# Performance work log

Hardware: AMD Instinct MI355X
Metric: run time of the kernel (lower is better)

## Reference

```python
import jax, jax.numpy as jnp
import numpy as np

L, D, H, V, T_MAX, DFF = 8, 1024, 16, 50257, 1024, 4096
HS = D // H
EPS = 1e-5


def setup_inputs() -> dict:
    key = jax.random.key(0)
    ks = jax.random.split(key, 20)
    s = 0.02
    inp = {
        "idx": jax.random.randint(ks[0], (4, 1024), 0, V),
        "wte": jax.random.normal(ks[1], (V, D), jnp.float32) * s,
        "wpe": jax.random.normal(ks[2], (T_MAX, D), jnp.float32) * s,
        "wq": jax.random.normal(ks[3], (L, D, D), jnp.float32) * s,
        "wk": jax.random.normal(ks[4], (L, D, D), jnp.float32) * s,
        "wv": jax.random.normal(ks[5], (L, D, D), jnp.float32) * s,
        "wo": jax.random.normal(ks[6], (L, D, D), jnp.float32) * s,
        "bo": jnp.zeros((L, D), jnp.float32),
        "ln1_w": jnp.ones((L, D), jnp.float32),
        "ln1_b": jnp.zeros((L, D), jnp.float32),
        "ln2_w": jnp.ones((L, D), jnp.float32),
        "ln2_b": jnp.zeros((L, D), jnp.float32),
        "w1": jax.random.normal(ks[7], (L, D, DFF), jnp.float32) * s,
        "b1": jnp.zeros((L, DFF), jnp.float32),
        "w2": jax.random.normal(ks[8], (L, DFF, D), jnp.float32) * s,
        "b2": jnp.zeros((L, D), jnp.float32),
        "lnf_w": jnp.ones((D,), jnp.float32),
        "lnf_b": jnp.zeros((D,), jnp.float32),
        "wlm": jax.random.normal(ks[9], (D, V), jnp.float32) * s,
        "blm": jnp.zeros((V,), jnp.float32),
    }
    return inp


def _ln(x, w, b):
    mu = jnp.mean(x, axis=-1, keepdims=True)
    var = jnp.mean(jnp.square(x - mu), axis=-1, keepdims=True)
    return (x - mu) * jax.lax.rsqrt(var + EPS) * w + b


def _gpt_forward(idx, wte, wpe, wq, wk, wv, wo, bo, ln1_w, ln1_b, ln2_w, ln2_b,
                 w1, b1, w2, b2, lnf_w, lnf_b, wlm, blm):
    B, T = idx.shape
    x = wte[idx] + wpe[:T]                       # [B,T,D]
    causal = jnp.tril(jnp.ones((T, T), bool))    # same as tril buffer
    scale = HS ** -0.5
    for i in range(L):
        h = _ln(x, ln1_w[i], ln1_b[i])
        q = (h @ wq[i]).reshape(B, T, H, HS)
        k = (h @ wk[i]).reshape(B, T, H, HS)
        v = (h @ wv[i]).reshape(B, T, H, HS)
        wei = jnp.einsum('bqhd,bkhd->bhqk', q, k) * scale
        wei = jnp.where(causal, wei, -jnp.inf)
        wei = jax.nn.softmax(wei, axis=-1)
        attn = jnp.einsum('bhqk,bkhd->bqhd', wei, v).reshape(B, T, D)
        x = x + attn @ wo[i] + bo[i]
        h2 = _ln(x, ln2_w[i], ln2_b[i])
        x = x + jax.nn.relu(h2 @ w1[i] + b1[i]) @ w2[i] + b2[i]
    x = _ln(x, lnf_w, lnf_b)
    return x @ wlm + blm                          # logits [B,T,V]


def reference(idx, wte, wpe, wq, wk, wv, wo, bo, ln1_w, ln1_b, ln2_w, ln2_b,
              w1, b1, w2, b2, lnf_w, lnf_b, wlm, blm):
    return _gpt_forward(idx, wte, wpe, wq, wk, wv, wo, bo, ln1_w, ln1_b,
                        ln2_w, ln2_b, w1, b1, w2, b2, lnf_w, lnf_b, wlm, blm)
```

## Files before the change

kernel.cpp:

```cpp
#include <hip/hip_runtime.h>
#include <cstdint>
#include <cstddef>

typedef __attribute__((ext_vector_type(4))) float f32x4;
typedef __attribute__((ext_vector_type(8))) short s16x8;
typedef __attribute__((ext_vector_type(4))) unsigned short u16x4;
typedef __attribute__((ext_vector_type(2))) unsigned short u16x2;

#define NLAYER 8
#define DM 1024
#define NTOK 4096
#define DFF2 4096
#define NV 50257

__device__ __forceinline__ unsigned short f2bf(float f) {
  unsigned int u = __float_as_uint(f);
  u = u + 0x7fffu + ((u >> 16) & 1u);
  return (unsigned short)(u >> 16);
}

__device__ __forceinline__ void gload_lds16(const void* gp, void* lp) {
  const __attribute__((address_space(1))) unsigned int* g =
      reinterpret_cast<const __attribute__((address_space(1))) unsigned int*>(
          reinterpret_cast<uintptr_t>(gp));
  __attribute__((address_space(3))) unsigned int* l =
      reinterpret_cast<__attribute__((address_space(3))) unsigned int*>(
          (unsigned int)(uintptr_t)lp);
  __builtin_amdgcn_global_load_lds(g, l, 16, 0, 0);
}

__global__ void __launch_bounds__(256) convT_k(const float* __restrict__ in,
                                               unsigned short* __restrict__ out,
                                               int K, int N, size_t zStride) {
  __shared__ float tile[64][65];
  const int n0 = blockIdx.x * 64, k0 = blockIdx.y * 64;
  const float* inp = in + (size_t)blockIdx.z * K * N;
  unsigned short* outp = out + (size_t)blockIdx.z * zStride;
  const int tid = threadIdx.x;
#pragma unroll
  for (int p = 0; p < 16; ++p) {
    const int r = p * 4 + (tid >> 6);
    const int cc = tid & 63;
    const int gn = n0 + cc;
    tile[r][cc] = (gn < N) ? inp[(size_t)(k0 + r) * N + gn] : 0.f;
  }
  __syncthreads();
#pragma unroll
  for (int p = 0; p < 8; ++p) {
    const int lin = p * 256 + tid;
    const int rn = lin >> 5;
    const int c2 = (lin & 31) * 2;
    u16x2 o;
    o[0] = f2bf(tile[c2][rn]);
    o[1] = f2bf(tile[c2 + 1][rn]);
    *(u16x2*)&outp[(size_t)(n0 + rn) * K + k0 + c2] = o;
  }
}

__global__ void __launch_bounds__(256) embed_k(const int* __restrict__ idx,
                                               const float* __restrict__ wte,
                                               const float* __restrict__ wpe,
                                               float* __restrict__ X) {
  const int tok = blockIdx.x;
  const int t = tok & 1023;
  const int id = idx[tok];
  const int c = threadIdx.x * 4;
  f32x4 a = *(const f32x4*)&wte[(size_t)id * DM + c];
  f32x4 p = *(const f32x4*)&wpe[(size_t)t * DM + c];
  a = a + p;
  *(f32x4*)&X[(size_t)tok * DM + c] = a;
}

__global__ void __launch_bounds__(256) ln_k(const float* __restrict__ X,
                                            const float* __restrict__ W,
                                            const float* __restrict__ Bp,
                                            unsigned short* __restrict__ O) {
  const int row = blockIdx.x, tid = threadIdx.x;
  const size_t base = (size_t)row * DM;
  f32x4 v = *(const f32x4*)&X[base + tid * 4];
  float s = v[0] + v[1] + v[2] + v[3];
  float q = v[0] * v[0] + v[1] * v[1] + v[2] * v[2] + v[3] * v[3];
#pragma unroll
  for (int m = 1; m < 64; m <<= 1) {
    s += __shfl_xor(s, m);
    q += __shfl_xor(q, m);
  }
  __shared__ float ps[4], pq[4];
  const int wv = tid >> 6;
  if ((tid & 63) == 0) { ps[wv] = s; pq[wv] = q; }
  __syncthreads();
  s = ps[0] + ps[1] + ps[2] + ps[3];
  q = pq[0] + pq[1] + pq[2] + pq[3];
  const float mu = s * (1.f / DM);
  const float var = q * (1.f / DM) - mu * mu;
  const float rstd = rsqrtf(var + 1e-5f);
  f32x4 w = *(const f32x4*)&W[tid * 4];
  f32x4 bb = *(const f32x4*)&Bp[tid * 4];
  u16x4 o;
#pragma unroll
  for (int j = 0; j < 4; ++j) o[j] = f2bf((v[j] - mu) * rstd * w[j] + bb[j]);
  *(u16x4*)&O[base + tid * 4] = o;
}

__global__ void __launch_bounds__(256) reduce2ln_k(
    float* __restrict__ X, const float* __restrict__ bias,
    const float* __restrict__ P0, const float* __restrict__ P1,
    const float* __restrict__ W, const float* __restrict__ Bp,
    unsigned short* __restrict__ O) {
  const int row = blockIdx.x, tid = threadIdx.x;
  const size_t base = (size_t)row * DM;
  const size_t i = base + tid * 4;
  f32x4 v = *(f32x4*)&X[i];
  {
    f32x4 b = *(const f32x4*)&bias[tid * 4];
    f32x4 a = *(const f32x4*)&P0[i];
    f32x4 c = *(const f32x4*)&P1[i];
    v = v + b + a + c;
    *(f32x4*)&X[i] = v;
  }
  float s = v[0] + v[1] + v[2] + v[3];
  float q = v[0] * v[0] + v[1] * v[1] + v[2] * v[2] + v[3] * v[3];
#pragma unroll
  for (int m = 1; m < 64; m <<= 1) {
    s += __shfl_xor(s, m);
    q += __shfl_xor(q, m);
  }
  __shared__ float ps[4], pq[4];
  const int wv = tid >> 6;
  if ((tid & 63) == 0) { ps[wv] = s; pq[wv] = q; }
  __syncthreads();
  s = ps[0] + ps[1] + ps[2] + ps[3];
  q = pq[0] + pq[1] + pq[2] + pq[3];
  const float mu = s * (1.f / DM);
  const float var = q * (1.f / DM) - mu * mu;
  const float rstd = rsqrtf(var + 1e-5f);
  f32x4 w = *(const f32x4*)&W[tid * 4];
  f32x4 bb = *(const f32x4*)&Bp[tid * 4];
  u16x4 o;
#pragma unroll
  for (int j = 0; j < 4; ++j) o[j] = f2bf((v[j] - mu) * rstd * w[j] + bb[j]);
  *(u16x4*)&O[base + tid * 4] = o;
}

__global__ void __launch_bounds__(256) gemm_k(
    const unsigned short* __restrict__ A, const unsigned short* __restrict__ Bt,
    const float* __restrict__ bias, float* __restrict__ outF,
    unsigned short* __restrict__ outB, int M, int N, int K, int lda, int ldc) {
  __shared__ __align__(16) unsigned short lA[128 * 64];
  __shared__ __align__(16) unsigned short lB[128 * 64];
  const int tid = threadIdx.x;
  const int wv = tid >> 6, lane = tid & 63;
  const int row0 = blockIdx.y * 128, col0 = blockIdx.x * 128;
  const int wr = wv >> 1, wc = wv & 1;

  const int z = blockIdx.z;
  A += (size_t)z * K;
  Bt += (size_t)z * K;
  if (gridDim.z > 1) outF += (size_t)z * M * ldc;

  f32x4 acc[4][4] = {};

  const int sRow = tid >> 3;
  const int sColSw = ((tid & 7) * 8) ^ ((sRow & 7) * 8);
  const unsigned short* gA = A + (size_t)(row0 + sRow) * lda + sColSw;
  const unsigned short* gB = Bt + (size_t)(col0 + sRow) * lda + sColSw;
  unsigned short* lAd = lA + tid * 8;
  unsigned short* lBd = lB + tid * 8;
  const size_t step32 = (size_t)32 * lda;

  const int rbase = lane & 15;
  const int kHi = (lane >> 4) * 8;
  const int kSw = (lane & 7) * 8;

  for (int kt = 0; kt < K; kt += 64) {
#pragma unroll
    for (int i = 0; i < 4; ++i) {
      gload_lds16(gA + kt + i * step32, lAd + i * 2048);
      gload_lds16(gB + kt + i * step32, lBd + i * 2048);
    }
    __syncthreads();
    s16x8 af[2][4], bfr[2][4];
#pragma unroll
    for (int kk = 0; kk < 2; ++kk) {
      const int kph = (kk * 32 + kHi) ^ kSw;
#pragma unroll
      for (int m = 0; m < 4; ++m)
        af[kk][m] = *(const s16x8*)&lA[(wr * 64 + m * 16 + rbase) * 64 + kph];
#pragma unroll
      for (int n = 0; n < 4; ++n)
        bfr[kk][n] = *(const s16x8*)&lB[(wc * 64 + n * 16 + rbase) * 64 + kph];
    }
#pragma unroll
    for (int kk = 0; kk < 2; ++kk)
#pragma unroll
      for (int m = 0; m < 4; ++m)
#pragma unroll
        for (int n = 0; n < 4; ++n)
          acc[m][n] = __builtin_amdgcn_mfma_f32_16x16x32_bf16(
              af[kk][m], bfr[kk][n], acc[m][n], 0, 0, 0);
    __syncthreads();
  }

  const int baseRow = row0 + wr * 64 + ((lane >> 4) * 4);
  const int baseCol = col0 + wc * 64 + (lane & 15);
#pragma unroll
  for (int m = 0; m < 4; ++m) {
#pragma unroll
    for (int n = 0; n < 4; ++n) {
      const int colc = baseCol + n * 16;
      if (colc < N) {
        const float bv = bias ? bias[colc] : 0.f;
        const int rowc0 = baseRow + m * 16;
#pragma unroll
        for (int r = 0; r < 4; ++r) {
          float v = acc[m][n][r] + bv;
          if (outF) outF[(size_t)(rowc0 + r) * ldc + colc] = v;
          if (outB) outB[(size_t)(rowc0 + r) * ldc + colc] = f2bf(v);
        }
      }
    }
  }
}

__global__ void __launch_bounds__(512, 2) gemm8p_k(
    const unsigned short* __restrict__ A, const unsigned short* __restrict__ Bt,
    const float* __restrict__ bias, float* __restrict__ outF,
    unsigned short* __restrict__ outB, unsigned short* __restrict__ vt,
    int M, int N, int K, int lda, int ldc, int relu) {
  __shared__ __align__(16) unsigned short lA[2][2][8192];
  __shared__ __align__(16) unsigned short lB[2][2][8192];
  const int tid = threadIdx.x;
  const int wv = tid >> 6, lane = tid & 63;

  int bx = blockIdx.x, by = blockIdx.y;
  {
    const int nwg = gridDim.x * gridDim.y;
    if ((nwg & 7) == 0) {
      int lin = by * gridDim.x + bx;
      lin = (lin & 7) * (nwg >> 3) + (lin >> 3);
      by = lin / gridDim.x;
      bx = lin - by * gridDim.x;
    }
  }
  const int row0 = by * 256, col0 = bx * 256;
  const int wr = wv >> 2, wc = wv & 3;

  f32x4 acc[8][4] = {};

  const int sColSw = (((tid & 7) ^ ((tid >> 3) & 7))) * 8;
  const unsigned short* gA = A + (size_t)(row0 + (tid >> 3)) * lda + sColSw;
  const unsigned short* gB = Bt + (size_t)(col0 + (tid >> 3)) * lda + sColSw;
  const size_t step64 = (size_t)64 * lda;

  const int rbase = lane & 15;
  const int g8 = (lane >> 4) * 8;
  const int rsw = (rbase & 7) * 8;

  const int nt = K >> 6;

#define STGA(t, h)                                                       \
  {                                                                      \
    const unsigned short* s_ = gA + (size_t)(t) * 64 + (size_t)(2 * (h)) * step64; \
    gload_lds16(s_, &lA[(t) & 1][h][tid * 8]);                           \
    gload_lds16(s_ + step64, &lA[(t) & 1][h][4096 + tid * 8]);           \
  }
#define STGB(t, h)                                                       \
  {                                                                      \
    const unsigned short* s_ = gB + (size_t)(t) * 64 + (size_t)(2 * (h)) * step64; \
    gload_lds16(s_, &lB[(t) & 1][h][tid * 8]);                           \
    gload_lds16(s_ + step64, &lB[(t) & 1][h][4096 + tid * 8]);           \
  }

  STGA(0, 0); STGA(0, 1); STGB(0, 0); STGB(0, 1);
  STGA(1, 0); STGA(1, 1); STGB(1, 0);
  asm volatile("s_waitcnt vmcnt(6)" ::: "memory");
  __builtin_amdgcn_s_barrier();

  for (int t = 0; t < nt; ++t) {
    const int d = t & 1;
    const unsigned short* lah = &lA[d][wr][0];
    const unsigned short* lbh = &lB[d][wc >> 1][0];
    const int bro = (wc & 1) * 64;
    s16x8 af0[4][2], af1[4][2], bf01[2][2], bf23[2][2];
#pragma unroll
    for (int ks = 0; ks < 2; ++ks) {
      const int kph = (ks * 32 + g8) ^ rsw;
#pragma unroll
      for (int m = 0; m < 4; ++m)
        af0[m][ks] = *(const s16x8*)&lah[(m * 16 + rbase) * 64 + kph];
#pragma unroll
      for (int n = 0; n < 2; ++n)
        bf01[n][ks] = *(const s16x8*)&lbh[(bro + n * 16 + rbase) * 64 + kph];
    }
    if (t + 1 < nt) STGB(t + 1, 1);
    __builtin_amdgcn_s_barrier();
    asm volatile("s_waitcnt lgkmcnt(0)" ::: "memory");
    __builtin_amdgcn_s_setprio(1);
#pragma unroll
    for (int m = 0; m < 4; ++m)
#pragma unroll
      for (int n = 0; n < 2; ++n)
#pragma unroll
        for (int ks = 0; ks < 2; ++ks)
          acc[m][n] = __builtin_amdgcn_mfma_f32_16x16x32_bf16(
              af0[m][ks], bf01[n][ks], acc[m][n], 0, 0, 0);
    __builtin_amdgcn_s_setprio(0);
    __builtin_amdgcn_s_barrier();
#pragma unroll
    for (int ks = 0; ks < 2; ++ks) {
      const int kph = (ks * 32 + g8) ^ rsw;
#pragma unroll
      for (int m = 0; m < 4; ++m)
        af1[m][ks] = *(const s16x8*)&lah[(64 + m * 16 + rbase) * 64 + kph];
    }
    __builtin_amdgcn_s_barrier();
    asm volatile("s_waitcnt lgkmcnt(0)" ::: "memory");
    __builtin_amdgcn_s_setprio(1);
#pragma unroll
    for (int m = 0; m < 4; ++m)
#pragma unroll
      for (int n = 0; n < 2; ++n)
#pragma unroll
        for (int ks = 0; ks < 2; ++ks)
          acc[4 + m][n] = __builtin_amdgcn_mfma_f32_16x16x32_bf16(
              af1[m][ks], bf01[n][ks], acc[4 + m][n], 0, 0, 0);
    __builtin_amdgcn_s_setprio(0);
    __builtin_amdgcn_s_barrier();
#pragma unroll
    for (int ks = 0; ks < 2; ++ks) {
      const int kph = (ks * 32 + g8) ^ rsw;
#pragma unroll
      for (int n = 0; n < 2; ++n)
        bf23[n][ks] =
            *(const s16x8*)&lbh[(bro + 32 + n * 16 + rbase) * 64 + kph];
    }
    if (t + 2 < nt) STGA(t + 2, 0);
    __builtin_amdgcn_s_barrier();
    asm volatile("s_waitcnt lgkmcnt(0)" ::: "memory");
    __builtin_amdgcn_s_setprio(1);
#pragma unroll
    for (int m = 0; m < 4; ++m)
#pragma unroll
      for (int n = 0; n < 2; ++n)
#pragma unroll
        for (int ks = 0; ks < 2; ++ks)
          acc[m][2 + n] = __builtin_amdgcn_mfma_f32_16x16x32_bf16(
              af0[m][ks], bf23[n][ks], acc[m][2 + n], 0, 0, 0);
    __builtin_amdgcn_s_setprio(0);
    __builtin_amdgcn_s_barrier();
    if (t + 2 < nt) { STGA(t + 2, 1); STGB(t + 2, 0); }
    __builtin_amdgcn_s_setprio(1);
#pragma unroll
    for (int m = 0; m < 4; ++m)
#pragma unroll
      for (int n = 0; n < 2; ++n)
#pragma unroll
        for (int ks = 0; ks < 2; ++ks)
          acc[4 + m][2 + n] = __builtin_amdgcn_mfma_f32_16x16x32_bf16(
              af1[m][ks], bf23[n][ks], acc[4 + m][2 + n], 0, 0, 0);
    __builtin_amdgcn_s_setprio(0);
    if (t + 2 < nt)
      asm volatile("s_waitcnt vmcnt(6)" ::: "memory");
    else if (t + 1 < nt)
      asm volatile("s_waitcnt vmcnt(0)" ::: "memory");
    __builtin_amdgcn_s_barrier();
  }
#undef STGA
#undef STGB

  const int baseRow = row0 + wr * 128 + ((lane >> 4) * 4);
  const int baseCol = col0 + wc * 64 + rbase;
#pragma unroll
  for (int m = 0; m < 8; ++m) {
#pragma unroll
    for (int n = 0; n < 4; ++n) {
      const int colc = baseCol + n * 16;
      if (colc < N) {
        const int rowc0 = baseRow + m * 16;
        if (vt && colc >= 2048) {
          const int f = colc - 2048;
          const int b = rowc0 >> 10, t0 = rowc0 & 1023;
          u16x4 o;
#pragma unroll
          for (int r = 0; r < 4; ++r) o[r] = f2bf(acc[m][n][r]);
          *(u16x4*)&vt[((size_t)((b << 4) + (f >> 6)) * 64 + (f & 63)) * 1024 + t0] = o;
        } else {
          const float bv = bias ? bias[colc] : 0.f;
#pragma unroll
          for (int r = 0; r < 4; ++r) {
            float v = acc[m][n][r] + bv;
            if (relu) v = fmaxf(v, 0.f);
            if (outF) outF[(size_t)(rowc0 + r) * ldc + colc] = v;
            if (outB) outB[(size_t)(rowc0 + r) * ldc + colc] = f2bf(v);
          }
        }
      }
    }
  }
}

__global__ void __launch_bounds__(256) attn_k(const unsigned short* __restrict__ Q,
                                              const unsigned short* __restrict__ Kb,
                                              const unsigned short* __restrict__ Vt,
                                              unsigned short* __restrict__ O,
                                              int ldq) {
  const int qt = blockIdx.x;
  const int bh = blockIdx.y;
  const int b = bh >> 4, h = bh & 15;
  const int tid = threadIdx.x, wv = tid >> 6, lane = tid & 63;
  const int g = lane >> 4, c = lane & 15;
  __shared__ __align__(16) unsigned short lP[4][2][16 * 64];
  const int qw0 = qt * 64 + wv * 16;
  s16x8 qf0, qf1;
  {
    const size_t qoff = ((size_t)(b * 1024 + qw0 + c)) * ldq + h * 64 + g * 8;
    qf0 = *(const s16x8*)&Q[qoff];
    qf1 = *(const s16x8*)&Q[qoff + 32];
  }
  f32x4 acc[4] = {};
  float lsum[4] = {0.f, 0.f, 0.f, 0.f};
  const float SC = 0.18033688011f;
  const float SB = -5.77078016356f;

  auto tile = [&](int kt, bool diag) {
    const int pb = kt & 1;
    unsigned short* lp = &lP[wv][pb][0];
    float p[4][4];
#pragma unroll
    for (int n = 0; n < 4; ++n) {
      if (diag && n > wv) {
#pragma unroll
        for (int r = 0; r < 4; ++r) p[n][r] = 0.f;
        continue;
      }
      f32x4 s = {};
      const size_t koff =
          ((size_t)(b * 1024 + kt * 64 + n * 16 + c)) * ldq + h * 64 + g * 8;
      s16x8 k0 = *(const s16x8*)&Kb[koff];
      s16x8 k1 = *(const s16x8*)&Kb[koff + 32];
      s = __builtin_amdgcn_mfma_f32_16x16x32_bf16(qf0, k0, s, 0, 0, 0);
      s = __builtin_amdgcn_mfma_f32_16x16x32_bf16(qf1, k1, s, 0, 0, 0);
      if (diag && n == wv) {
#pragma unroll
        for (int r = 0; r < 4; ++r) {
          const float e = (c > g * 4 + r) ? 0.f : exp2f(fmaf(s[r], SC, SB));
          p[n][r] = e;
          lsum[r] += e;
        }
      } else {
#pragma unroll
        for (int r = 0; r < 4; ++r) {
          const float e = exp2f(fmaf(s[r], SC, SB));
          p[n][r] = e;
          lsum[r] += e;
        }
      }
    }
#pragma unroll
    for (int n = 0; n < 4; ++n)
#pragma unroll
      for (int r = 0; r < 4; ++r)
        lp[(g * 4 + r) * 64 + n * 16 + c] = f2bf(p[n][r]);
    s16x8 pa0 = *(const s16x8*)&lp[c * 64 + g * 8];
    s16x8 pa1 = *(const s16x8*)&lp[c * 64 + 32 + g * 8];
#pragma unroll
    for (int n = 0; n < 4; ++n) {
      const size_t voff =
          ((size_t)(bh * 64 + n * 16 + c)) * 1024 + kt * 64 + g * 8;
      s16x8 v0 = *(const s16x8*)&Vt[voff];
      s16x8 v1 = *(const s16x8*)&Vt[voff + 32];
      acc[n] = __builtin_amdgcn_mfma_f32_16x16x32_bf16(pa0, v0, acc[n], 0, 0, 0);
      acc[n] = __builtin_amdgcn_mfma_f32_16x16x32_bf16(pa1, v1, acc[n], 0, 0, 0);
    }
  };

  for (int kt = 0; kt < qt; ++kt) tile(kt, false);
  tile(qt, true);

  float inv[4];
#pragma unroll
  for (int r = 0; r < 4; ++r) {
#pragma unroll
    for (int m = 1; m <= 8; m <<= 1) lsum[r] += __shfl_xor(lsum[r], m);
    inv[r] = 1.f / lsum[r];
  }
#pragma unroll
  for (int n = 0; n < 4; ++n)
#pragma unroll
    for (int r = 0; r < 4; ++r) {
      const size_t row = (size_t)(b * 1024 + qw0 + g * 4 + r);
      O[row * DM + h * 64 + n * 16 + c] = f2bf(acc[n][r] * inv[r]);
    }
}

extern "C" void kernel_launch(void* const* d_in, const int* in_sizes, int n_in,
                              void* d_out, int out_size, void* d_ws, size_t ws_size,
                              hipStream_t stream) {
  const int* idx = (const int*)d_in[0];
  const float* wte = (const float*)d_in[1];
  const float* wpe = (const float*)d_in[2];
  const float* wq = (const float*)d_in[3];
  const float* wk = (const float*)d_in[4];
  const float* wv = (const float*)d_in[5];
  const float* wo = (const float*)d_in[6];
  const float* bo = (const float*)d_in[7];
  const float* ln1w = (const float*)d_in[8];
  const float* ln1b = (const float*)d_in[9];
  const float* ln2w = (const float*)d_in[10];
  const float* ln2b = (const float*)d_in[11];
  const float* w1 = (const float*)d_in[12];
  const float* b1 = (const float*)d_in[13];
  const float* w2 = (const float*)d_in[14];
  const float* b2 = (const float*)d_in[15];
  const float* lnfw = (const float*)d_in[16];
  const float* lnfb = (const float*)d_in[17];
  const float* wlm = (const float*)d_in[18];
  const float* blm = (const float*)d_in[19];
  float* out = (float*)d_out;

  char* ws = (char*)d_ws;
  size_t off = 0;
  auto alloc = [&](size_t bytes) -> void* {
    void* p = ws + off;
    off += (bytes + 255) & ~(size_t)255;
    return p;
  };
  unsigned short* wqkvT = (unsigned short*)alloc((size_t)NLAYER * 3072 * DM * 2);
  unsigned short* woT = (unsigned short*)alloc((size_t)NLAYER * DM * DM * 2);
  unsigned short* w1T = (unsigned short*)alloc((size_t)NLAYER * DM * DFF2 * 2);
  unsigned short* w2T = (unsigned short*)alloc((size_t)NLAYER * DM * DFF2 * 2);
  unsigned short* wlmT = w1T;
  float* X = (float*)alloc((size_t)NTOK * DM * 4);
  unsigned short* Hb = (unsigned short*)alloc((size_t)NTOK * DM * 2);
  char* uni = (char*)alloc((size_t)32 * 1024 * 1024);
  unsigned short* QKVb = (unsigned short*)uni;
  unsigned short* Ab = (unsigned short*)(uni + (size_t)24 * 1024 * 1024);
  float* P0 = (float*)uni;
  float* P1 = (float*)(uni + (size_t)16 * 1024 * 1024);
  unsigned short* VtB = (unsigned short*)alloc((size_t)NTOK * DM * 2);
  unsigned short* Mid = (unsigned short*)alloc((size_t)NTOK * DFF2 * 2);
  float* MidF = (float*)Mid;

  const size_t qkvStride = (size_t)3072 * DM;
  convT_k<<<dim3(16, 16, 8), 256, 0, stream>>>(wq, wqkvT, DM, DM, qkvStride);
  convT_k<<<dim3(16, 16, 8), 256, 0, stream>>>(wk, wqkvT + (size_t)1024 * DM, DM, DM, qkvStride);
  convT_k<<<dim3(16, 16, 8), 256, 0, stream>>>(wv, wqkvT + (size_t)2048 * DM, DM, DM, qkvStride);
  convT_k<<<dim3(16, 16, 8), 256, 0, stream>>>(wo, woT, DM, DM, (size_t)DM * DM);
  convT_k<<<dim3(64, 16, 8), 256, 0, stream>>>(w1, w1T, DM, DFF2, (size_t)DM * DFF2);
  convT_k<<<dim3(16, 64, 8), 256, 0, stream>>>(w2, w2T, DFF2, DM, (size_t)DM * DFF2);

  embed_k<<<dim3(NTOK), 256, 0, stream>>>(idx, wte, wpe, X);
  ln_k<<<dim3(NTOK), 256, 0, stream>>>(X, ln1w, ln1b, Hb);

  for (int i = 0; i < NLAYER; ++i) {
    const size_t wOff = (size_t)i * DM * DM;
    const size_t fOff = (size_t)i * DM * DFF2;
    gemm8p_k<<<dim3(12, 16), 512, 0, stream>>>(Hb, wqkvT + i * qkvStride,
                                               nullptr, nullptr, QKVb, VtB,
                                               NTOK, 3072, DM, DM, 3072, 0);
    attn_k<<<dim3(16, 64), 256, 0, stream>>>(QKVb, QKVb + 1024, VtB, Ab, 3072);
    gemm_k<<<dim3(8, 32, 2), 256, 0, stream>>>(Ab, woT + wOff, nullptr, MidF,
                                               nullptr, NTOK, DM, DM / 2, DM, DM);
    reduce2ln_k<<<dim3(NTOK), 256, 0, stream>>>(X, bo + i * DM, MidF,
                                                MidF + (size_t)NTOK * DM,
                                                ln2w + i * DM, ln2b + i * DM, Hb);
    gemm8p_k<<<dim3(16, 16), 512, 0, stream>>>(Hb, w1T + fOff, b1 + i * DFF2,
                                               nullptr, Mid, nullptr, NTOK,
                                               DFF2, DM, DM, DFF2, 1);
    gemm_k<<<dim3(8, 32, 2), 256, 0, stream>>>(Mid, w2T + fOff, nullptr, P0,
                                               nullptr, NTOK, DM, DFF2 / 2,
                                               DFF2, DM);
    const float* nw = (i < NLAYER - 1) ? ln1w + (i + 1) * DM : lnfw;
    const float* nb = (i < NLAYER - 1) ? ln1b + (i + 1) * DM : lnfb;
    reduce2ln_k<<<dim3(NTOK), 256, 0, stream>>>(X, b2 + i * DM, P0, P1, nw, nb, Hb);
  }

  convT_k<<<dim3(788, 16, 1), 256, 0, stream>>>(wlm, wlmT, DM, NV, 0);
  gemm8p_k<<<dim3(197, 16), 512, 0, stream>>>(Hb, wlmT, blm, out, nullptr,
                                              nullptr, NTOK, NV, DM, DM, NV, 0);
}
```

Measured before the change: 3.257 ms.

## Process two query tiles per attention block to reuse K/V loads

Each attention block now handles 128 query rows (two 64-row tiles) instead of 64, so every K and V fragment loaded from global memory feeds both tiles' MFMAs. The grid is halved to 8x64 blocks, and diagonal masking is handled per tile through mode flags. This cuts K/V global traffic per query, at the cost of higher register pressure (two sets of accumulators and probabilities), fewer blocks in flight, and a heavier per-block causal load imbalance.

```diff
diff --git a/kernel.cpp b/kernel.cpp
--- a/kernel.cpp
+++ b/kernel.cpp
@@ -409,87 +409,136 @@
   const int b = bh >> 4, h = bh & 15;
   const int tid = threadIdx.x, wv = tid >> 6, lane = tid & 63;
   const int g = lane >> 4, c = lane & 15;
-  __shared__ __align__(16) unsigned short lP[4][2][16 * 64];
-  const int qw0 = qt * 64 + wv * 16;
-  s16x8 qf0, qf1;
+  __shared__ __align__(16) unsigned short lP[4][2][2][16 * 64];
+  const int qb0 = qt * 128 + wv * 16;
+  const int qb1 = qb0 + 64;
+  s16x8 qfA0, qfA1, qfB0, qfB1;
   {
-    const size_t qoff = ((size_t)(b * 1024 + qw0 + c)) * ldq + h * 64 + g * 8;
-    qf0 = *(const s16x8*)&Q[qoff];
-    qf1 = *(const s16x8*)&Q[qoff + 32];
-  }
-  f32x4 acc[4] = {};
-  float lsum[4] = {0.f, 0.f, 0.f, 0.f};
+    const size_t qoffA = ((size_t)(b * 1024 + qb0 + c)) * ldq + h * 64 + g * 8;
+    qfA0 = *(const s16x8*)&Q[qoffA];
+    qfA1 = *(const s16x8*)&Q[qoffA + 32];
+    const size_t qoffB = ((size_t)(b * 1024 + qb1 + c)) * ldq + h * 64 + g * 8;
+    qfB0 = *(const s16x8*)&Q[qoffB];
+    qfB1 = *(const s16x8*)&Q[qoffB + 32];
+  }
+  f32x4 accA[4] = {}, accB[4] = {};
+  float lsumA[4] = {0.f, 0.f, 0.f, 0.f}, lsumB[4] = {0.f, 0.f, 0.f, 0.f};
   const float SC = 0.18033688011f;
   const float SB = -5.77078016356f;
 
-  auto tile = [&](int kt, bool diag) {
+  const int nt = 2 * qt + 2;
+  for (int kt = 0; kt < nt; ++kt) {
+    const int modeA = (kt < nt - 2) ? 0 : ((kt == nt - 2) ? 1 : 2);
+    const int modeB = (kt < nt - 1) ? 0 : 1;
     const int pb = kt & 1;
-    unsigned short* lp = &lP[wv][pb][0];
-    float p[4][4];
+    unsigned short* lpA = &lP[wv][pb][0][0];
+    unsigned short* lpB = &lP[wv][pb][1][0];
+    float pA[4][4], pB[4][4];
 #pragma unroll
     for (int n = 0; n < 4; ++n) {
-      if (diag && n > wv) {
-#pragma unroll
-        for (int r = 0; r < 4; ++r) p[n][r] = 0.f;
-        continue;
-      }
-      f32x4 s = {};
       const size_t koff =
           ((size_t)(b * 1024 + kt * 64 + n * 16 + c)) * ldq + h * 64 + g * 8;
       s16x8 k0 = *(const s16x8*)&Kb[koff];
       s16x8 k1 = *(const s16x8*)&Kb[koff + 32];
-      s = __builtin_amdgcn_mfma_f32_16x16x32_bf16(qf0, k0, s, 0, 0, 0);
-      s = __builtin_amdgcn_mfma_f32_16x16x32_bf16(qf1, k1, s, 0, 0, 0);
-      if (diag && n == wv) {
-#pragma unroll
-        for (int r = 0; r < 4; ++r) {
-          const float e = (c > g * 4 + r) ? 0.f : exp2f(fmaf(s[r], SC, SB));
-          p[n][r] = e;
-          lsum[r] += e;
-        }
+      if (modeA == 2 || (modeA == 1 && n > wv)) {
+#pragma unroll
+        for (int r = 0; r < 4; ++r) pA[n][r] = 0.f;
       } else {
-#pragma unroll
-        for (int r = 0; r < 4; ++r) {
-          const float e = exp2f(fmaf(s[r], SC, SB));
-          p[n][r] = e;
-          lsum[r] += e;
+        f32x4 s = {};
+        s = __builtin_amdgcn_mfma_f32_16x16x32_bf16(qfA0, k0, s, 0, 0, 0);
+        s = __builtin_amdgcn_mfma_f32_16x16x32_bf16(qfA1, k1, s, 0, 0, 0);
+        if (modeA == 1 && n == wv) {
+#pragma unroll
+          for (int r = 0; r < 4; ++r) {
+            const float e = (c > g * 4 + r) ? 0.f : exp2f(fmaf(s[r], SC, SB));
+            pA[n][r] = e;
+            lsumA[r] += e;
+          }
+        } else {
+#pragma unroll
+          for (int r = 0; r < 4; ++r) {
+            const float e = exp2f(fmaf(s[r], SC, SB));
+            pA[n][r] = e;
+            lsumA[r] += e;
+          }
         }
       }
+      if (modeB == 1 && n > wv) {
+#pragma unroll
+        for (int r = 0; r < 4; ++r) pB[n][r] = 0.f;
+      } else {
+        f32x4 s = {};
+        s = __builtin_amdgcn_mfma_f32_16x16x32_bf16(qfB0, k0, s, 0, 0, 0);
+        s = __builtin_amdgcn_mfma_f32_16x16x32_bf16(qfB1, k1, s, 0, 0, 0);
+        if (modeB == 1 && n == wv) {
+#pragma unroll
+          for (int r = 0; r < 4; ++r) {
+            const float e = (c > g * 4 + r) ? 0.f : exp2f(fmaf(s[r], SC, SB));
+            pB[n][r] = e;
+            lsumB[r] += e;
+          }
+        } else {
+#pragma unroll
+          for (int r = 0; r < 4; ++r) {
+            const float e = exp2f(fmaf(s[r], SC, SB));
+            pB[n][r] = e;
+            lsumB[r] += e;
+          }
+        }
+      }
+    }
+    if (modeA < 2) {
+#pragma unroll
+      for (int n = 0; n < 4; ++n)
+#pragma unroll
+        for (int r = 0; r < 4; ++r)
+          lpA[(g * 4 + r) * 64 + n * 16 + c] = f2bf(pA[n][r]);
     }
 #pragma unroll
     for (int n = 0; n < 4; ++n)
 #pragma unroll
       for (int r = 0; r < 4; ++r)
-        lp[(g * 4 + r) * 64 + n * 16 + c] = f2bf(p[n][r]);
-    s16x8 pa0 = *(const s16x8*)&lp[c * 64 + g * 8];
-    s16x8 pa1 = *(const s16x8*)&lp[c * 64 + 32 + g * 8];
+        lpB[(g * 4 + r) * 64 + n * 16 + c] = f2bf(pB[n][r]);
+    s16x8 paA0, paA1;
+    if (modeA < 2) {
+      paA0 = *(const s16x8*)&lpA[c * 64 + g * 8];
+      paA1 = *(const s16x8*)&lpA[c * 64 + 32 + g * 8];
+    }
+    s16x8 paB0 = *(const s16x8*)&lpB[c * 64 + g * 8];
+    s16x8 paB1 = *(const s16x8*)&lpB[c * 64 + 32 + g * 8];
 #pragma unroll
     for (int n = 0; n < 4; ++n) {
       const size_t voff =
           ((size_t)(bh * 64 + n * 16 + c)) * 1024 + kt * 64 + g * 8;
       s16x8 v0 = *(const s16x8*)&Vt[voff];
       s16x8 v1 = *(const s16x8*)&Vt[voff + 32];
-      acc[n] = __builtin_amdgcn_mfma_f32_16x16x32_bf16(pa0, v0, acc[n], 0, 0, 0);
-      acc[n] = __builtin_amdgcn_mfma_f32_16x16x32_bf16(pa1, v1, acc[n], 0, 0, 0);
-    }
-  };
-
-  for (int kt = 0; kt < qt; ++kt) tile(kt, false);
-  tile(qt, true);
-
-  float inv[4];
+      if (modeA < 2) {
+        accA[n] = __builtin_amdgcn_mfma_f32_16x16x32_bf16(paA0, v0, accA[n], 0, 0, 0);
+        accA[n] = __builtin_amdgcn_mfma_f32_16x16x32_bf16(paA1, v1, accA[n], 0, 0, 0);
+      }
+      accB[n] = __builtin_amdgcn_mfma_f32_16x16x32_bf16(paB0, v0, accB[n], 0, 0, 0);
+      accB[n] = __builtin_amdgcn_mfma_f32_16x16x32_bf16(paB1, v1, accB[n], 0, 0, 0);
+    }
+  }
+  float invA[4], invB[4];
 #pragma unroll
   for (int r = 0; r < 4; ++r) {
 #pragma unroll
-    for (int m = 1; m <= 8; m <<= 1) lsum[r] += __shfl_xor(lsum[r], m);
-    inv[r] = 1.f / lsum[r];
+    for (int m = 1; m <= 8; m <<= 1) {
+      lsumA[r] += __shfl_xor(lsumA[r], m);
+      lsumB[r] += __shfl_xor(lsumB[r], m);
+    }
+    invA[r] = 1.f / lsumA[r];
+    invB[r] = 1.f / lsumB[r];
   }
 #pragma unroll
   for (int n = 0; n < 4; ++n)
 #pragma unroll
     for (int r = 0; r < 4; ++r) {
-      const size_t row = (size_t)(b * 1024 + qw0 + g * 4 + r);
-      O[row * DM + h * 64 + n * 16 + c] = f2bf(acc[n][r] * inv[r]);
+      const size_t rowA = (size_t)(b * 1024 + qb0 + g * 4 + r);
+      O[rowA * DM + h * 64 + n * 16 + c] = f2bf(accA[n][r] * invA[r]);
+      const size_t rowB = (size_t)(b * 1024 + qb1 + g * 4 + r);
+      O[rowB * DM + h * 64 + n * 16 + c] = f2bf(accB[n][r] * invB[r]);
     }
 }
 
@@ -558,7 +607,7 @@
     gemm8p_k<<<dim3(12, 16), 512, 0, stream>>>(Hb, wqkvT + i * qkvStride,
                                                nullptr, nullptr, QKVb, VtB,
                                                NTOK, 3072, DM, DM, 3072, 0);
-    attn_k<<<dim3(16, 64), 256, 0, stream>>>(QKVb, QKVb + 1024, VtB, Ab, 3072);
+    attn_k<<<dim3(8, 64), 256, 0, stream>>>(QKVb, QKVb + 1024, VtB, Ab, 3072);
     gemm_k<<<dim3(8, 32, 2), 256, 0, stream>>>(Ab, woT + wOff, nullptr, MidF,
                                                nullptr, NTOK, DM, DM / 2, DM, DM);
     reduce2ln_k<<<dim3(NTOK), 256, 0, stream>>>(X, bo + i * DM, MidF,
```

Result: faster. 2.941 ms (-9.7%).
